# Kernel tuning notes

Hardware: AMD Instinct MI355X
Metric: run time of the kernel (lower is better)

The kernel has to match this reference:

```python
import jax, jax.numpy as jnp
import numpy as np

IN_F = 1024
OUT_F = 1024

def setup_inputs() -> dict:
    key = jax.random.key(0)
    k1, k2, k3, k4, k5 = jax.random.split(key, 5)
    B, S = 64, 512
    bound_W = 1.0 / np.sqrt(OUT_F)
    bound_U = 1.0 / np.sqrt(IN_F)
    return {
        "input_emb": jax.random.normal(k1, (B, S, IN_F), dtype=jnp.float32),
        "W_w": jax.random.uniform(k2, (OUT_F, OUT_F), jnp.float32, -bound_W, bound_W),
        "W_b": jax.random.uniform(k3, (OUT_F,), jnp.float32, -bound_W, bound_W),
        "U_w": jax.random.uniform(k4, (OUT_F, IN_F), jnp.float32, -bound_U, bound_U),
        "U_b": jax.random.uniform(k5, (OUT_F,), jnp.float32, -bound_U, bound_U),
    }

def reference(input_emb, W_w, W_b, U_w, U_b):
    B = input_emb.shape[0]
    # Precompute input projection for all timesteps: [B,S,H]
    Ux = jnp.einsum('bsi,hi->bsh', input_emb, U_w) + U_b
    h0 = jnp.zeros((B, OUT_F), dtype=input_emb.dtype)

    def step(h_p, ux_t):
        h = jnp.tanh(ux_t + h_p @ W_w.T + W_b)
        return h, h

    h_last, outs = jax.lax.scan(step, h0, jnp.swapaxes(Ux, 0, 1))  # outs: [S,B,H]
    outputs = jnp.swapaxes(outs, 0, 1)  # [B,S,H]
    return outputs, h_last
```

## Files before the change

kernel.cpp:

```cpp
#include <hip/hip_runtime.h>
#include <hip/hip_bf16.h>

#define SEQ 512
#define NB  64
#define HF  1024

typedef float f32x4 __attribute__((ext_vector_type(4)));
typedef short s16x8 __attribute__((ext_vector_type(8)));
typedef short s16x4 __attribute__((ext_vector_type(4)));
typedef _Float16 f16x8 __attribute__((ext_vector_type(8)));
typedef unsigned long long u64;

__device__ __forceinline__ unsigned short bf16_rne(float f) {
    unsigned u = __builtin_bit_cast(unsigned, f);
    u += 0x7FFFu + ((u >> 16) & 1u);
    return (unsigned short)(u >> 16);
}

__device__ __forceinline__ void bf16_split(float f, short& hi, short& lo) {
    unsigned u = __builtin_bit_cast(unsigned, f);
    hi = (short)(u >> 16);
    float fh = __builtin_bit_cast(float, u & 0xFFFF0000u);
    lo = (short)bf16_rne(f - fh);
}

__device__ __forceinline__ f32x4 mfma16(s16x8 a, s16x8 b, f32x4 c) {
    return __builtin_amdgcn_mfma_f32_16x16x32_bf16(a, b, c, 0, 0, 0);
}

__device__ __forceinline__ f32x4 mfma16f(f16x8 a, f16x8 b, f32x4 c) {
    return __builtin_amdgcn_mfma_f32_16x16x32_f16(a, b, c, 0, 0, 0);
}

__global__ __launch_bounds__(256, 2) void ux_gemm(const float* __restrict__ X,
                                                  const float* __restrict__ U,
                                                  const float* __restrict__ Ubias,
                                                  float* __restrict__ out) {
    __shared__ short Ah[128][40], Al[128][40], Bh[128][40], Bl[128][40];

    int bid = blockIdx.x;
    int swz = (bid & 7) * 256 + (bid >> 3);
    int tm = swz & 255;
    int tn = swz >> 8;

    int tid  = threadIdx.x;
    int lrow = tid >> 3;
    int lcol = (tid & 7) << 2;

    int wave = tid >> 6, lane = tid & 63;
    int wr = (wave >> 1) << 6;
    int wc = (wave & 1) << 6;
    int fr = lane & 15, fkq = lane >> 4;

    const float* Xb = X + (size_t)tm * 128 * HF;
    const float* Ub = U + (size_t)tn * 128 * HF;

    f32x4 acc[4][4];
    #pragma unroll
    for (int mi = 0; mi < 4; ++mi)
        #pragma unroll
        for (int ni = 0; ni < 4; ++ni)
            acc[mi][ni] = f32x4{0.f, 0.f, 0.f, 0.f};

    for (int kt = 0; kt < HF; kt += 32) {
        __syncthreads();
        #pragma unroll
        for (int p = 0; p < 4; ++p) {
            int r = lrow + (p << 5);
            f32x4 xv = *(const f32x4*)(Xb + (size_t)r * HF + kt + lcol);
            f32x4 uv = *(const f32x4*)(Ub + (size_t)r * HF + kt + lcol);
            s16x4 xh, xl, uh, ul;
            #pragma unroll
            for (int e = 0; e < 4; ++e) {
                short h_, l_;
                bf16_split(xv[e], h_, l_); xh[e] = h_; xl[e] = l_;
                bf16_split(uv[e], h_, l_); uh[e] = h_; ul[e] = l_;
            }
            *(s16x4*)&Ah[r][lcol] = xh;
            *(s16x4*)&Al[r][lcol] = xl;
            *(s16x4*)&Bh[r][lcol] = uh;
            *(s16x4*)&Bl[r][lcol] = ul;
        }
        __syncthreads();

        s16x8 afh[4], afl[4], bfh[4], bfl[4];
        #pragma unroll
        for (int mi = 0; mi < 4; ++mi) {
            afh[mi] = *(const s16x8*)&Ah[wr + mi * 16 + fr][fkq * 8];
            afl[mi] = *(const s16x8*)&Al[wr + mi * 16 + fr][fkq * 8];
            bfh[mi] = *(const s16x8*)&Bh[wc + mi * 16 + fr][fkq * 8];
            bfl[mi] = *(const s16x8*)&Bl[wc + mi * 16 + fr][fkq * 8];
        }
        #pragma unroll
        for (int mi = 0; mi < 4; ++mi)
            #pragma unroll
            for (int ni = 0; ni < 4; ++ni)
                acc[mi][ni] = mfma16(afh[mi], bfh[ni], acc[mi][ni]);
        #pragma unroll
        for (int mi = 0; mi < 4; ++mi)
            #pragma unroll
            for (int ni = 0; ni < 4; ++ni)
                acc[mi][ni] = mfma16(afh[mi], bfl[ni], acc[mi][ni]);
        #pragma unroll
        for (int mi = 0; mi < 4; ++mi)
            #pragma unroll
            for (int ni = 0; ni < 4; ++ni)
                acc[mi][ni] = mfma16(afl[mi], bfh[ni], acc[mi][ni]);
    }

    #pragma unroll
    for (int ni = 0; ni < 4; ++ni) {
        int col = tn * 128 + wc + ni * 16 + fr;
        float ub = Ubias[col];
        #pragma unroll
        for (int mi = 0; mi < 4; ++mi) {
            #pragma unroll
            for (int i = 0; i < 4; ++i) {
                int row = tm * 128 + wr + mi * 16 + fkq * 4 + i;
                out[(size_t)row * HF + col] = acc[mi][ni][i] + ub;
            }
        }
    }
}

__global__ __launch_bounds__(512, 2) void rnn_scan(const float* __restrict__ Ww,
                                                   const float* __restrict__ Wb,
                                                   float* __restrict__ out,
                                                   _Float16* __restrict__ hb,
                                                   unsigned int* __restrict__ flags) {
    __shared__ _Float16 Hs[16 * HF];

    int bid   = blockIdx.x;
    int btile = bid >> 3;
    int wgidx = bid & 7;
    int tid   = threadIdx.x;
    int wave  = tid >> 6, lane = tid & 63;
    int fr    = lane & 15, fkq = lane >> 4;
    int j     = ((wgidx * 8 + wave) << 4) + fr;
    int b0    = btile << 4;
    int xr    = (fr & 7) << 4;

    f16x8 wf[32];
    {
        const float* wp = Ww + (size_t)j * HF + fkq * 8;
        #pragma unroll
        for (int kt = 0; kt < 32; ++kt) {
            f32x4 a = *(const f32x4*)(wp + kt * 32);
            f32x4 b = *(const f32x4*)(wp + kt * 32 + 4);
            f16x8 w;
            #pragma unroll
            for (int e = 0; e < 4; ++e) {
                w[e]     = (_Float16)a[e];
                w[e + 4] = (_Float16)b[e];
            }
            wf[kt] = w;
        }
    }
    float wb = Wb[j];

    unsigned int* grp_flags = flags + btile * 16;

    #pragma unroll 1
    for (int t = 0; t < SEQ; ++t) {
        float ux[4];
        #pragma unroll
        for (int i = 0; i < 4; ++i) {
            int r = b0 + fkq * 4 + i;
            ux[i] = out[((size_t)r * SEQ + t) * HF + j];
        }

        f32x4 sum = {0.f, 0.f, 0.f, 0.f};
        if (t > 0) {
            unsigned int v;
            do {
                v = (lane < 8)
                    ? __hip_atomic_load(&grp_flags[lane], __ATOMIC_RELAXED,
                                        __HIP_MEMORY_SCOPE_AGENT)
                    : 0xFFFFFFFFu;
            } while (!__all(v >= (unsigned int)t));

            int par = (t - 1) & 1;
            const u64* src = (const u64*)(hb + ((size_t)par * NB + b0) * HF);
            #pragma unroll
            for (int k = 0; k < 4; ++k) {
                int c = (k << 9) + tid;
                u64 a0 = __hip_atomic_load(src + c * 2,     __ATOMIC_RELAXED,
                                           __HIP_MEMORY_SCOPE_AGENT);
                u64 a1 = __hip_atomic_load(src + c * 2 + 1, __ATOMIC_RELAXED,
                                           __HIP_MEMORY_SCOPE_AGENT);
                *(u64*)((char*)Hs + c * 16)     = a0;
                *(u64*)((char*)Hs + c * 16 + 8) = a1;
            }
            __syncthreads();

            f32x4 a0 = {0.f,0.f,0.f,0.f}, a1 = a0, a2 = a0, a3 = a0;
            int rbase = fr << 11;
            #pragma unroll
            for (int kt = 0; kt < 32; ++kt) {
                int boff = (fkq * 16 + (kt << 6)) ^ xr;
                f16x8 hv = *(const f16x8*)((const char*)Hs + rbase + boff);
                if ((kt & 3) == 0)      a0 = mfma16f(hv, wf[kt], a0);
                else if ((kt & 3) == 1) a1 = mfma16f(hv, wf[kt], a1);
                else if ((kt & 3) == 2) a2 = mfma16f(hv, wf[kt], a2);
                else                    a3 = mfma16f(hv, wf[kt], a3);
            }
            sum = (a0 + a1) + (a2 + a3);
        }

        int par_w = t & 1;
        char* hrow = (char*)(hb + (size_t)par_w * NB * HF);
        #pragma unroll
        for (int i = 0; i < 4; ++i) {
            int lr = fkq * 4 + i;
            int r  = b0 + lr;
            float p = ux[i] + sum[i] + wb;
            p = fminf(fmaxf(p, -12.f), 12.f);
            float e2 = __expf(2.f * p);
            float h  = (e2 - 1.f) / (e2 + 1.f);
            out[((size_t)r * SEQ + t) * HF + j] = h;
            if (t == SEQ - 1)
                out[(size_t)NB * SEQ * HF + (size_t)r * HF + j] = h;
            _Float16 hf = (_Float16)h;
            size_t boff = (size_t)r * 2048 + (size_t)((j * 2) ^ ((lr & 7) << 4));
            __hip_atomic_store((short*)(hrow + boff),
                               __builtin_bit_cast(short, hf),
                               __ATOMIC_RELAXED, __HIP_MEMORY_SCOPE_AGENT);
        }

        asm volatile("s_waitcnt vmcnt(0)" ::: "memory");
        __syncthreads();
        if (tid == 0) {
            __hip_atomic_store(&grp_flags[wgidx], (unsigned int)(t + 1),
                               __ATOMIC_RELAXED, __HIP_MEMORY_SCOPE_AGENT);
        }
    }
}

extern "C" void kernel_launch(void* const* d_in, const int* in_sizes, int n_in,
                              void* d_out, int out_size, void* d_ws, size_t ws_size,
                              hipStream_t stream) {
    const float* X  = (const float*)d_in[0];
    const float* Ww = (const float*)d_in[1];
    const float* Wb = (const float*)d_in[2];
    const float* Uw = (const float*)d_in[3];
    const float* Ub = (const float*)d_in[4];
    float* out = (float*)d_out;

    unsigned int* flags = (unsigned int*)d_ws;
    _Float16* hb = (_Float16*)((char*)d_ws + 8192);

    hipMemsetAsync(d_ws, 0, 8192, stream);
    ux_gemm<<<dim3(2048), dim3(256), 0, stream>>>(X, Uw, Ub, out);
    rnn_scan<<<dim3(32), dim3(512), 0, stream>>>(Ww, Wb, out, hb, flags);
}
```

Measured before the change: 2.524 ms.

## Load hidden state straight into registers and move output stores off the critical path

The recurrent step no longer stages the previous hidden state through shared memory with a barrier. Each lane now loads its MFMA operand fragments directly from global memory, double-buffered in blocks of eight k-tiles, and the swizzled layout is dropped. The output stores and the next step's Ux loads now run after the flag publish, so the s_waitcnt before the flag covers only the hidden-state stores and the Ux load latency overlaps the next wait. The trade-off is more register pressure and redundant global/L2 reads, since each wave now fetches the full 16x1024 tile itself.

```diff
diff --git a/kernel.cpp b/kernel.cpp
--- a/kernel.cpp
+++ b/kernel.cpp
@@ -10,6 +10,7 @@
 typedef short s16x4 __attribute__((ext_vector_type(4)));
 typedef _Float16 f16x8 __attribute__((ext_vector_type(8)));
 typedef unsigned long long u64;
+typedef u64 u64x2 __attribute__((ext_vector_type(2)));
 
 __device__ __forceinline__ unsigned short bf16_rne(float f) {
     unsigned u = __builtin_bit_cast(unsigned, f);
@@ -32,6 +33,10 @@
     return __builtin_amdgcn_mfma_f32_16x16x32_f16(a, b, c, 0, 0, 0);
 }
 
+__device__ __forceinline__ u64 ald(const u64* p) {
+    return __hip_atomic_load(p, __ATOMIC_RELAXED, __HIP_MEMORY_SCOPE_AGENT);
+}
+
 __global__ __launch_bounds__(256, 2) void ux_gemm(const float* __restrict__ X,
                                                   const float* __restrict__ U,
                                                   const float* __restrict__ Ubias,
@@ -128,8 +133,6 @@
                                                    float* __restrict__ out,
                                                    _Float16* __restrict__ hb,
                                                    unsigned int* __restrict__ flags) {
-    __shared__ _Float16 Hs[16 * HF];
-
     int bid   = blockIdx.x;
     int btile = bid >> 3;
     int wgidx = bid & 7;
@@ -138,7 +141,6 @@
     int fr    = lane & 15, fkq = lane >> 4;
     int j     = ((wgidx * 8 + wave) << 4) + fr;
     int b0    = btile << 4;
-    int xr    = (fr & 7) << 4;
 
     f16x8 wf[32];
     {
@@ -160,15 +162,15 @@
 
     unsigned int* grp_flags = flags + btile * 16;
 
+    float ux[4];
+    #pragma unroll
+    for (int i = 0; i < 4; ++i) {
+        int r = b0 + fkq * 4 + i;
+        ux[i] = out[((size_t)r * SEQ + 0) * HF + j];
+    }
+
     #pragma unroll 1
     for (int t = 0; t < SEQ; ++t) {
-        float ux[4];
-        #pragma unroll
-        for (int i = 0; i < 4; ++i) {
-            int r = b0 + fkq * 4 + i;
-            ux[i] = out[((size_t)r * SEQ + t) * HF + j];
-        }
-
         f32x4 sum = {0.f, 0.f, 0.f, 0.f};
         if (t > 0) {
             unsigned int v;
@@ -180,49 +182,52 @@
             } while (!__all(v >= (unsigned int)t));
 
             int par = (t - 1) & 1;
-            const u64* src = (const u64*)(hb + ((size_t)par * NB + b0) * HF);
-            #pragma unroll
-            for (int k = 0; k < 4; ++k) {
-                int c = (k << 9) + tid;
-                u64 a0 = __hip_atomic_load(src + c * 2,     __ATOMIC_RELAXED,
-                                           __HIP_MEMORY_SCOPE_AGENT);
-                u64 a1 = __hip_atomic_load(src + c * 2 + 1, __ATOMIC_RELAXED,
-                                           __HIP_MEMORY_SCOPE_AGENT);
-                *(u64*)((char*)Hs + c * 16)     = a0;
-                *(u64*)((char*)Hs + c * 16 + 8) = a1;
-            }
-            __syncthreads();
-
+            const u64* lanep =
+                (const u64*)(hb + ((size_t)par * NB + b0 + fr) * HF + fkq * 8);
+            u64 bA[2][8], bB[2][8];
+            #pragma unroll
+            for (int q = 0; q < 8; ++q) {
+                bA[0][q] = ald(lanep + q * 8);
+                bB[0][q] = ald(lanep + q * 8 + 1);
+            }
             f32x4 a0 = {0.f,0.f,0.f,0.f}, a1 = a0, a2 = a0, a3 = a0;
-            int rbase = fr << 11;
-            #pragma unroll
-            for (int kt = 0; kt < 32; ++kt) {
-                int boff = (fkq * 16 + (kt << 6)) ^ xr;
-                f16x8 hv = *(const f16x8*)((const char*)Hs + rbase + boff);
-                if ((kt & 3) == 0)      a0 = mfma16f(hv, wf[kt], a0);
-                else if ((kt & 3) == 1) a1 = mfma16f(hv, wf[kt], a1);
-                else if ((kt & 3) == 2) a2 = mfma16f(hv, wf[kt], a2);
-                else                    a3 = mfma16f(hv, wf[kt], a3);
+            #pragma unroll
+            for (int blk = 0; blk < 4; ++blk) {
+                if (blk < 3) {
+                    #pragma unroll
+                    for (int q = 0; q < 8; ++q) {
+                        bA[(blk + 1) & 1][q] = ald(lanep + (blk + 1) * 64 + q * 8);
+                        bB[(blk + 1) & 1][q] = ald(lanep + (blk + 1) * 64 + q * 8 + 1);
+                    }
+                }
+                #pragma unroll
+                for (int q = 0; q < 8; ++q) {
+                    u64x2 pr;
+                    pr[0] = bA[blk & 1][q];
+                    pr[1] = bB[blk & 1][q];
+                    f16x8 hv = __builtin_bit_cast(f16x8, pr);
+                    int kt = blk * 8 + q;
+                    if ((q & 3) == 0)      a0 = mfma16f(hv, wf[kt], a0);
+                    else if ((q & 3) == 1) a1 = mfma16f(hv, wf[kt], a1);
+                    else if ((q & 3) == 2) a2 = mfma16f(hv, wf[kt], a2);
+                    else                   a3 = mfma16f(hv, wf[kt], a3);
+                }
             }
             sum = (a0 + a1) + (a2 + a3);
         }
 
+        float hv4[4];
         int par_w = t & 1;
-        char* hrow = (char*)(hb + (size_t)par_w * NB * HF);
         #pragma unroll
         for (int i = 0; i < 4; ++i) {
-            int lr = fkq * 4 + i;
-            int r  = b0 + lr;
+            int r = b0 + fkq * 4 + i;
             float p = ux[i] + sum[i] + wb;
             p = fminf(fmaxf(p, -12.f), 12.f);
             float e2 = __expf(2.f * p);
             float h  = (e2 - 1.f) / (e2 + 1.f);
-            out[((size_t)r * SEQ + t) * HF + j] = h;
-            if (t == SEQ - 1)
-                out[(size_t)NB * SEQ * HF + (size_t)r * HF + j] = h;
+            hv4[i] = h;
             _Float16 hf = (_Float16)h;
-            size_t boff = (size_t)r * 2048 + (size_t)((j * 2) ^ ((lr & 7) << 4));
-            __hip_atomic_store((short*)(hrow + boff),
+            __hip_atomic_store((short*)&hb[((size_t)par_w * NB + r) * HF + j],
                                __builtin_bit_cast(short, hf),
                                __ATOMIC_RELAXED, __HIP_MEMORY_SCOPE_AGENT);
         }
@@ -232,6 +237,21 @@
         if (tid == 0) {
             __hip_atomic_store(&grp_flags[wgidx], (unsigned int)(t + 1),
                                __ATOMIC_RELAXED, __HIP_MEMORY_SCOPE_AGENT);
+        }
+
+        #pragma unroll
+        for (int i = 0; i < 4; ++i) {
+            int r = b0 + fkq * 4 + i;
+            out[((size_t)r * SEQ + t) * HF + j] = hv4[i];
+            if (t == SEQ - 1)
+                out[(size_t)NB * SEQ * HF + (size_t)r * HF + j] = hv4[i];
+        }
+        if (t + 1 < SEQ) {
+            #pragma unroll
+            for (int i = 0; i < 4; ++i) {
+                int r = b0 + fkq * 4 + i;
+                ux[i] = out[((size_t)r * SEQ + (t + 1)) * HF + j];
+            }
         }
     }
 }
```

New measurement: 8.513 ms. 237% more time.
